# Kernel optimization log

Measured on AMD Instinct MI355X. Metric: run time of the kernel, lower is better.

The kernel has to match this reference:

```python
import jax, jax.numpy as jnp
import numpy as np

N, IN_DIM, OUT_DIM = 16384, 256, 128

def setup_inputs() -> dict:
    key = jax.random.key(0)
    ks = jax.random.split(key, 7)
    s_in = 1.0 / np.sqrt(IN_DIM)
    return {
        "x": jax.random.normal(ks[0], (N, IN_DIM), dtype=jnp.float32),
        "Wq": jax.random.uniform(ks[1], (IN_DIM, OUT_DIM), jnp.float32, -s_in, s_in),
        "bq": jax.random.uniform(ks[2], (OUT_DIM,), jnp.float32, -s_in, s_in),
        "Wk": jax.random.uniform(ks[3], (IN_DIM, OUT_DIM), jnp.float32, -s_in, s_in),
        "bk": jax.random.uniform(ks[4], (OUT_DIM,), jnp.float32, -s_in, s_in),
        "Wv": jax.random.uniform(ks[5], (IN_DIM, OUT_DIM), jnp.float32, -s_in, s_in),
        "bv": jax.random.uniform(ks[6], (OUT_DIM,), jnp.float32, -s_in, s_in),
    }

def reference(x, Wq, bq, Wk, bk, Wv, bv):
    # QKV projections: [N, out_dim]
    q = x @ Wq + bq
    k = x @ Wk + bk
    v = x @ Wv + bv
    # Unscaled dot-product affinity [N, N], row softmax, weighted sum of V.
    affinity = jax.nn.softmax(q @ k.T, axis=-1)
    return affinity @ v
```

## Files before the change

### kernel.cpp

```cpp
#include <hip/hip_runtime.h>

typedef _Float16 f16;
typedef _Float16 f16x8 __attribute__((ext_vector_type(8)));
typedef float f32x4 __attribute__((ext_vector_type(4)));
typedef float f32x16 __attribute__((ext_vector_type(16)));
typedef unsigned uint2v __attribute__((ext_vector_type(2)));

#define MFMA16(a, b, c) __builtin_amdgcn_mfma_f32_16x16x32_f16((a), (b), (c), 0, 0, 0)
#define MFMA32(a, b, c) __builtin_amdgcn_mfma_f32_32x32x16_f16((a), (b), (c), 0, 0, 0)
#define LOG2E 1.44269504088896340736f
#define SHIFT_L2 28.8539008178f

#define GLOAD_LDS16(g, l)                                              \
    __builtin_amdgcn_global_load_lds(                                  \
        (const __attribute__((address_space(1))) void*)(g),            \
        (__attribute__((address_space(3))) void*)(l), 16, 0, 0)

#define NROWS 16384
#define INDIM 256
#define ODIM 128
#define NQT 128

__global__ __launch_bounds__(256) void prep_kernel(
    const float* __restrict__ Wq, const float* __restrict__ Wk, const float* __restrict__ Wv,
    f16* __restrict__ WqT, f16* __restrict__ WkT, f16* __restrict__ WvT) {
    int w = blockIdx.x >> 5;
    int local = blockIdx.x & 31;
    const float* W = (w == 0) ? Wq : ((w == 1) ? Wk : Wv);
    f16* WT = (w == 0) ? WqT : ((w == 1) ? WkT : WvT);
    int j0 = local * 1024 + threadIdx.x;
#pragma unroll
    for (int t = 0; t < 4; t++) {
        int j = j0 + t * 256;
        int n = j >> 8;
        int k = j & 255;
        WT[j] = (f16)W[k * ODIM + n];
    }
}

__global__ __launch_bounds__(256) void proj_kernel(
    const float* __restrict__ x,
    const f16* __restrict__ WqT, const f16* __restrict__ WkT, const f16* __restrict__ WvT,
    const float* __restrict__ bq, const float* __restrict__ bk, const float* __restrict__ bv,
    f16* __restrict__ Qh, f16* __restrict__ Kh, f16* __restrict__ Vt) {
    int blk = blockIdx.x;
    int wave = threadIdx.x >> 6;
    int lane = threadIdx.x & 63;
    int l16 = lane & 15, quad = lane >> 4;

    int r0 = (blk & 255) * 64 + wave * 16;
    int c0 = (blk >> 8) * 64;

    f16x8 ax[8];
    const float* xp = x + (size_t)(r0 + l16) * INDIM + quad * 8;
#pragma unroll
    for (int kc = 0; kc < 8; kc++) {
        f32x4 u = *(const f32x4*)(xp + kc * 32);
        f32x4 v = *(const f32x4*)(xp + kc * 32 + 4);
        f16x8 t;
        t[0] = (f16)u[0]; t[1] = (f16)u[1]; t[2] = (f16)u[2]; t[3] = (f16)u[3];
        t[4] = (f16)v[0]; t[5] = (f16)v[1]; t[6] = (f16)v[2]; t[7] = (f16)v[3];
        ax[kc] = t;
    }
#pragma unroll
    for (int nt = 0; nt < 4; nt++) {
        int colb = c0 + nt * 16;
        f32x4 aq = {0.f, 0.f, 0.f, 0.f}, ak = {0.f, 0.f, 0.f, 0.f};
        f32x4 av = {0.f, 0.f, 0.f, 0.f};
        const f16* wq = WqT + (colb + l16) * INDIM + quad * 8;
        const f16* wk = WkT + (colb + l16) * INDIM + quad * 8;
        const f16* wv = WvT + (colb + l16) * INDIM + quad * 8;
#pragma unroll
        for (int kc = 0; kc < 8; kc++) {
            f16x8 bqf = *(const f16x8*)(wq + kc * 32);
            f16x8 bkf = *(const f16x8*)(wk + kc * 32);
            f16x8 avf = *(const f16x8*)(wv + kc * 32);
            aq = MFMA16(ax[kc], bqf, aq);
            ak = MFMA16(ax[kc], bkf, ak);
            av = MFMA16(avf, ax[kc], av);
        }
        int col = colb + l16;
        float biasq = bq[col], biask = bk[col];
#pragma unroll
        for (int r = 0; r < 4; r++) {
            int row = r0 + quad * 4 + r;
            Qh[(size_t)row * ODIM + col] = (f16)(aq[r] + biasq);
            Kh[(size_t)row * ODIM + col] = (f16)(ak[r] + biask);
            int d = colb + quad * 4 + r;
            Vt[(size_t)d * NROWS + r0 + l16] = (f16)(av[r] + bv[d]);
        }
    }
}

__global__ __launch_bounds__(256, 2) void flash_kernel(
    const f16* __restrict__ Qh, const f16* __restrict__ Kh, const f16* __restrict__ Vt,
    float* __restrict__ Opart, float* __restrict__ lbuf, float* __restrict__ Out,
    int nsplit, int niter) {
    int blk = blockIdx.x;
    int qt = blk & (NQT - 1);
    int sp = blk >> 7;
    int tid = threadIdx.x;
    int wave = tid >> 6;
    int lane = tid & 63;
    int l32 = lane & 31;
    int h = lane >> 5;

    __shared__ __align__(16) f16 Kl[2][64 * 128];
    __shared__ __align__(16) f16 Vl[2][128 * 64];

    int rowbase = qt * 128 + wave * 32;

    f16x8 qf[8];
    {
        const f16* qp = Qh + (size_t)(rowbase + l32) * ODIM + h * 8;
#pragma unroll
        for (int ks = 0; ks < 8; ks++) qf[ks] = *(const f16x8*)(qp + ks * 16);
    }

    f32x16 o[4];
#pragma unroll
    for (int dt = 0; dt < 4; dt++)
#pragma unroll
        for (int g = 0; g < 16; g++) o[dt][g] = 0.f;
    float l_r = 0.f;

    int rK[4], cK[4], dV[4], cV[4];
#pragma unroll
    for (int t = 0; t < 4; t++) {
        int s = wave * 256 + t * 64 + lane;
        rK[t] = s >> 4;
        cK[t] = ((s & 15) ^ (rK[t] & 7)) * 8;
        dV[t] = s >> 3;
        cV[t] = ((s & 7) ^ (dV[t] & 7)) * 8;
    }
    int rr = (l32 >> 1) & 3;
    int hh = h ^ (l32 & 1);

    int j0 = sp * (niter * 64);

#pragma unroll
    for (int t = 0; t < 4; t++) {
        GLOAD_LDS16(Kh + (size_t)(j0 + rK[t]) * ODIM + cK[t],
                    &Kl[0][(wave * 4 + t) * 512]);
        GLOAD_LDS16(Vt + (size_t)dV[t] * NROWS + j0 + cV[t],
                    &Vl[0][(wave * 4 + t) * 512]);
    }
    __syncthreads();

    for (int it = 0; it < niter; ++it) {
        int p = it & 1;
        if (it + 1 < niter) {
            int jn = j0 + 64;
#pragma unroll
            for (int t = 0; t < 4; t++) {
                GLOAD_LDS16(Kh + (size_t)(jn + rK[t]) * ODIM + cK[t],
                            &Kl[1 - p][(wave * 4 + t) * 512]);
                GLOAD_LDS16(Vt + (size_t)dV[t] * NROWS + jn + cV[t],
                            &Vl[1 - p][(wave * 4 + t) * 512]);
            }
        }
        int pk[2][8];
#pragma unroll
        for (int ct = 0; ct < 2; ct++) {
            f32x16 st;
#pragma unroll
            for (int g = 0; g < 16; g++) st[g] = 0.f;
            const f16* kb = &Kl[p][(ct * 32 + l32) * 128 + hh * 8];
#pragma unroll
            for (int ks = 0; ks < 8; ks++) {
                f16x8 kf = *(const f16x8*)(kb + ((ks ^ rr) << 4));
                st = MFMA32(kf, qf[ks], st);
            }
#pragma unroll
            for (int w = 0; w < 8; w++) {
                float a = __builtin_amdgcn_exp2f(fmaf(st[2 * w], LOG2E, -SHIFT_L2));
                float b = __builtin_amdgcn_exp2f(fmaf(st[2 * w + 1], LOG2E, -SHIFT_L2));
                l_r += a + b;
                pk[ct][w] = __builtin_bit_cast(int, __builtin_amdgcn_cvt_pkrtz(a, b));
            }
        }
        f16x8 pf[4];
#if __has_builtin(__builtin_amdgcn_permlane32_swap)
#pragma unroll
        for (int ks = 0; ks < 4; ks++) {
            int ct = ks >> 1, b = (ks & 1) * 4;
            uint2v r02 = __builtin_amdgcn_permlane32_swap(
                (unsigned)pk[ct][b], (unsigned)pk[ct][b + 2], false, false);
            uint2v r13 = __builtin_amdgcn_permlane32_swap(
                (unsigned)pk[ct][b + 1], (unsigned)pk[ct][b + 3], false, false);
            union { unsigned i[4]; f16x8 v; } u;
            u.i[0] = r02.x;
            u.i[1] = r13.x;
            u.i[2] = r02.y;
            u.i[3] = r13.y;
            pf[ks] = u.v;
        }
#else
#pragma unroll
        for (int ks = 0; ks < 4; ks++) {
            int ct = ks >> 1, b = (ks & 1) * 4;
            int off0 = h ? pk[ct][b] : pk[ct][b + 2];
            int off1 = h ? pk[ct][b + 1] : pk[ct][b + 3];
            int R0 = __shfl_xor(off0, 32, 64);
            int R1 = __shfl_xor(off1, 32, 64);
            union { int i[4]; f16x8 v; } u;
            u.i[0] = h ? R0 : pk[ct][b];
            u.i[1] = h ? R1 : pk[ct][b + 1];
            u.i[2] = h ? pk[ct][b + 2] : R0;
            u.i[3] = h ? pk[ct][b + 3] : R1;
            pf[ks] = u.v;
        }
#endif
#pragma unroll
        for (int dt = 0; dt < 4; dt++) {
            const f16* vb = &Vl[p][(dt * 32 + l32) * 64 + hh * 8];
#pragma unroll
            for (int ks = 0; ks < 4; ks++) {
                f16x8 vf = *(const f16x8*)(vb + ((ks ^ rr) << 4));
                o[dt] = MFMA32(vf, pf[ks], o[dt]);
            }
        }
        __syncthreads();
        j0 += 64;
    }

    l_r += __shfl_xor(l_r, 32, 64);

    if (nsplit == 1) {
        float inv = 1.f / l_r;
        float* op = Out + (size_t)(rowbase + l32) * ODIM;
#pragma unroll
        for (int dt = 0; dt < 4; dt++)
#pragma unroll
            for (int gg = 0; gg < 4; gg++) {
                f32x4 v = {o[dt][4 * gg] * inv, o[dt][4 * gg + 1] * inv,
                           o[dt][4 * gg + 2] * inv, o[dt][4 * gg + 3] * inv};
                *(f32x4*)(op + dt * 32 + 8 * gg + 4 * h) = v;
            }
    } else {
        float* op = Opart + ((size_t)sp * NROWS + rowbase + l32) * ODIM;
#pragma unroll
        for (int dt = 0; dt < 4; dt++)
#pragma unroll
            for (int gg = 0; gg < 4; gg++) {
                f32x4 v = {o[dt][4 * gg], o[dt][4 * gg + 1],
                           o[dt][4 * gg + 2], o[dt][4 * gg + 3]};
                *(f32x4*)(op + dt * 32 + 8 * gg + 4 * h) = v;
            }
        if (lane < 32)
            lbuf[(size_t)sp * NROWS + rowbase + l32] = l_r;
    }
}

__global__ __launch_bounds__(256) void merge_kernel(const float* __restrict__ Opart,
                                                    const float* __restrict__ lbuf,
                                                    float* __restrict__ out, int nsplit) {
    int idx = (blockIdx.x * 256 + threadIdx.x) * 4;
    int row = idx >> 7;
    f32x4 acc = {0.f, 0.f, 0.f, 0.f};
    float den = 0.f;
    for (int s = 0; s < nsplit; s++) {
        f32x4 v = *(const f32x4*)(Opart + (size_t)s * (NROWS * ODIM) + idx);
        acc[0] += v[0]; acc[1] += v[1]; acc[2] += v[2]; acc[3] += v[3];
        den += lbuf[(size_t)s * NROWS + row];
    }
    float inv = 1.f / den;
    f32x4 r = {acc[0] * inv, acc[1] * inv, acc[2] * inv, acc[3] * inv};
    *(f32x4*)(out + idx) = r;
}

extern "C" void kernel_launch(void* const* d_in, const int* in_sizes, int n_in,
                              void* d_out, int out_size, void* d_ws, size_t ws_size,
                              hipStream_t stream) {
    const float* x  = (const float*)d_in[0];
    const float* Wq = (const float*)d_in[1];
    const float* bq = (const float*)d_in[2];
    const float* Wk = (const float*)d_in[3];
    const float* bk = (const float*)d_in[4];
    const float* Wv = (const float*)d_in[5];
    const float* bv = (const float*)d_in[6];
    float* out = (float*)d_out;
    char* ws = (char*)d_ws;

    const size_t WT_BYTES = (size_t)ODIM * INDIM * sizeof(f16);
    const size_t QKV_BYTES = (size_t)NROWS * ODIM * sizeof(f16);
    f16* WqT = (f16*)(ws);
    f16* WkT = (f16*)(ws + WT_BYTES);
    f16* WvT = (f16*)(ws + 2 * WT_BYTES);
    f16* Qh  = (f16*)(ws + 3 * WT_BYTES);
    f16* Kh  = (f16*)(ws + 3 * WT_BYTES + QKV_BYTES);
    f16* Vt  = (f16*)(ws + 3 * WT_BYTES + 2 * QKV_BYTES);
    size_t base = 3 * WT_BYTES + 3 * QKV_BYTES;

    const size_t OPART_BYTES = (size_t)NROWS * ODIM * sizeof(float);
    const size_t L_BYTES = (size_t)NROWS * sizeof(float);

    int nsplit = 1;
    if (ws_size >= base + 4 * (OPART_BYTES + L_BYTES)) nsplit = 4;
    else if (ws_size >= base + 2 * (OPART_BYTES + L_BYTES)) nsplit = 2;

    float* Opart = (float*)(ws + base);
    float* lbuf  = (float*)(ws + base + (size_t)nsplit * OPART_BYTES);

    prep_kernel<<<96, 256, 0, stream>>>(Wq, Wk, Wv, WqT, WkT, WvT);
    proj_kernel<<<512, 256, 0, stream>>>(x, WqT, WkT, WvT, bq, bk, bv, Qh, Kh, Vt);
    flash_kernel<<<NQT * nsplit, 256, 0, stream>>>(Qh, Kh, Vt, Opart, lbuf, out, nsplit,
                                                   (NROWS / 64) / nsplit);
    if (nsplit > 1)
        merge_kernel<<<(NROWS * ODIM) / 1024, 256, 0, stream>>>(Opart, lbuf, out, nsplit);
}
```

Baseline: 244.6 us.

## Fuse prep, projection, flash and merge into one cooperative persistent kernel

Combines the four kernel launches into a single cooperative mega-kernel of 512 blocks that uses grid-wide syncs between the weight-transpose, QKV-projection, split flash-attention and merge phases. The aim is to remove launch gaps and per-kernel tail effects. In exchange it depends on cooperative launch support and on all 512 blocks being co-resident at two blocks per CU. The shared LDS allocation and the launch bounds of the flash phase now also apply to the lighter phases. If the cooperative launch fails, it falls back to the separate kernels.

```diff
diff --git a/kernel.cpp b/kernel.cpp
--- a/kernel.cpp
+++ b/kernel.cpp
@@ -1,4 +1,5 @@
 #include <hip/hip_runtime.h>
+#include <hip/hip_cooperative_groups.h>
 
 typedef _Float16 f16;
 typedef _Float16 f16x8 __attribute__((ext_vector_type(8)));
@@ -21,31 +22,26 @@
 #define ODIM 128
 #define NQT 128
 
-__global__ __launch_bounds__(256) void prep_kernel(
+__device__ __forceinline__ void prep_body(int gidx,
     const float* __restrict__ Wq, const float* __restrict__ Wk, const float* __restrict__ Wv,
     f16* __restrict__ WqT, f16* __restrict__ WkT, f16* __restrict__ WvT) {
-    int w = blockIdx.x >> 5;
-    int local = blockIdx.x & 31;
-    const float* W = (w == 0) ? Wq : ((w == 1) ? Wk : Wv);
-    f16* WT = (w == 0) ? WqT : ((w == 1) ? WkT : WvT);
-    int j0 = local * 1024 + threadIdx.x;
-#pragma unroll
-    for (int t = 0; t < 4; t++) {
-        int j = j0 + t * 256;
-        int n = j >> 8;
-        int k = j & 255;
+    if (gidx < 3 * 32768) {
+        int m = gidx >> 15;
+        int j = gidx & 32767;
+        const float* W = (m == 0) ? Wq : ((m == 1) ? Wk : Wv);
+        f16* WT = (m == 0) ? WqT : ((m == 1) ? WkT : WvT);
+        int n = j >> 8, k = j & 255;
         WT[j] = (f16)W[k * ODIM + n];
     }
 }
 
-__global__ __launch_bounds__(256) void proj_kernel(
+__device__ __forceinline__ void proj_body(int blk, int tid,
     const float* __restrict__ x,
     const f16* __restrict__ WqT, const f16* __restrict__ WkT, const f16* __restrict__ WvT,
     const float* __restrict__ bq, const float* __restrict__ bk, const float* __restrict__ bv,
     f16* __restrict__ Qh, f16* __restrict__ Kh, f16* __restrict__ Vt) {
-    int blk = blockIdx.x;
-    int wave = threadIdx.x >> 6;
-    int lane = threadIdx.x & 63;
+    int wave = tid >> 6;
+    int lane = tid & 63;
     int l16 = lane & 15, quad = lane >> 4;
 
     int r0 = (blk & 255) * 64 + wave * 16;
@@ -92,21 +88,20 @@
     }
 }
 
-__global__ __launch_bounds__(256, 2) void flash_kernel(
+__device__ __forceinline__ void flash_body(int blk, int tid,
+    f16* Kl0, f16* Kl1, f16* Vl0, f16* Vl1,
     const f16* __restrict__ Qh, const f16* __restrict__ Kh, const f16* __restrict__ Vt,
     float* __restrict__ Opart, float* __restrict__ lbuf, float* __restrict__ Out,
     int nsplit, int niter) {
-    int blk = blockIdx.x;
     int qt = blk & (NQT - 1);
     int sp = blk >> 7;
-    int tid = threadIdx.x;
     int wave = tid >> 6;
     int lane = tid & 63;
     int l32 = lane & 31;
     int h = lane >> 5;
 
-    __shared__ __align__(16) f16 Kl[2][64 * 128];
-    __shared__ __align__(16) f16 Vl[2][128 * 64];
+    f16* KlB[2] = {Kl0, Kl1};
+    f16* VlB[2] = {Vl0, Vl1};
 
     int rowbase = qt * 128 + wave * 32;
 
@@ -141,9 +136,9 @@
 #pragma unroll
     for (int t = 0; t < 4; t++) {
         GLOAD_LDS16(Kh + (size_t)(j0 + rK[t]) * ODIM + cK[t],
-                    &Kl[0][(wave * 4 + t) * 512]);
+                    &KlB[0][(wave * 4 + t) * 512]);
         GLOAD_LDS16(Vt + (size_t)dV[t] * NROWS + j0 + cV[t],
-                    &Vl[0][(wave * 4 + t) * 512]);
+                    &VlB[0][(wave * 4 + t) * 512]);
     }
     __syncthreads();
 
@@ -154,9 +149,9 @@
 #pragma unroll
             for (int t = 0; t < 4; t++) {
                 GLOAD_LDS16(Kh + (size_t)(jn + rK[t]) * ODIM + cK[t],
-                            &Kl[1 - p][(wave * 4 + t) * 512]);
+                            &KlB[1 - p][(wave * 4 + t) * 512]);
                 GLOAD_LDS16(Vt + (size_t)dV[t] * NROWS + jn + cV[t],
-                            &Vl[1 - p][(wave * 4 + t) * 512]);
+                            &VlB[1 - p][(wave * 4 + t) * 512]);
             }
         }
         int pk[2][8];
@@ -165,7 +160,7 @@
             f32x16 st;
 #pragma unroll
             for (int g = 0; g < 16; g++) st[g] = 0.f;
-            const f16* kb = &Kl[p][(ct * 32 + l32) * 128 + hh * 8];
+            const f16* kb = &KlB[p][(ct * 32 + l32) * 128 + hh * 8];
 #pragma unroll
             for (int ks = 0; ks < 8; ks++) {
                 f16x8 kf = *(const f16x8*)(kb + ((ks ^ rr) << 4));
@@ -213,7 +208,7 @@
 #endif
 #pragma unroll
         for (int dt = 0; dt < 4; dt++) {
-            const f16* vb = &Vl[p][(dt * 32 + l32) * 64 + hh * 8];
+            const f16* vb = &VlB[p][(dt * 32 + l32) * 64 + hh * 8];
 #pragma unroll
             for (int ks = 0; ks < 4; ks++) {
                 f16x8 vf = *(const f16x8*)(vb + ((ks ^ rr) << 4));
@@ -252,10 +247,9 @@
     }
 }
 
-__global__ __launch_bounds__(256) void merge_kernel(const float* __restrict__ Opart,
-                                                    const float* __restrict__ lbuf,
-                                                    float* __restrict__ out, int nsplit) {
-    int idx = (blockIdx.x * 256 + threadIdx.x) * 4;
+__device__ __forceinline__ void merge_body(int idx, int nsplit,
+    const float* __restrict__ Opart, const float* __restrict__ lbuf,
+    float* __restrict__ out) {
     int row = idx >> 7;
     f32x4 acc = {0.f, 0.f, 0.f, 0.f};
     float den = 0.f;
@@ -267,6 +261,70 @@
     float inv = 1.f / den;
     f32x4 r = {acc[0] * inv, acc[1] * inv, acc[2] * inv, acc[3] * inv};
     *(f32x4*)(out + idx) = r;
+}
+
+__global__ __launch_bounds__(256, 2) void mega_kernel(
+    const float* __restrict__ x,
+    const float* __restrict__ Wq, const float* __restrict__ bq,
+    const float* __restrict__ Wk, const float* __restrict__ bk,
+    const float* __restrict__ Wv, const float* __restrict__ bv,
+    f16* WqT, f16* WkT, f16* WvT, f16* Qh, f16* Kh, f16* Vt,
+    float* Opart, float* lbuf, float* out) {
+    __shared__ __align__(16) f16 Kl[2][64 * 128];
+    __shared__ __align__(16) f16 Vl[2][128 * 64];
+
+    cooperative_groups::grid_group grid = cooperative_groups::this_grid();
+    int blk = blockIdx.x;
+    int tid = threadIdx.x;
+
+    prep_body(blk * 256 + tid, Wq, Wk, Wv, WqT, WkT, WvT);
+    __threadfence();
+    grid.sync();
+
+    proj_body(blk, tid, x, WqT, WkT, WvT, bq, bk, bv, Qh, Kh, Vt);
+    __threadfence();
+    grid.sync();
+
+    flash_body(blk, tid, Kl[0], Kl[1], Vl[0], Vl[1],
+               Qh, Kh, Vt, Opart, lbuf, out, 4, 64);
+    __threadfence();
+    grid.sync();
+
+#pragma unroll
+    for (int i = 0; i < 4; i++) {
+        int idx = (blk * 256 + tid) * 4 + i * (512 * 256 * 4);
+        merge_body(idx, 4, Opart, lbuf, out);
+    }
+}
+
+__global__ __launch_bounds__(256) void prep_kernel(
+    const float* __restrict__ Wq, const float* __restrict__ Wk, const float* __restrict__ Wv,
+    f16* __restrict__ WqT, f16* __restrict__ WkT, f16* __restrict__ WvT) {
+    prep_body(blockIdx.x * 256 + threadIdx.x, Wq, Wk, Wv, WqT, WkT, WvT);
+}
+
+__global__ __launch_bounds__(256) void proj_kernel(
+    const float* __restrict__ x,
+    const f16* __restrict__ WqT, const f16* __restrict__ WkT, const f16* __restrict__ WvT,
+    const float* __restrict__ bq, const float* __restrict__ bk, const float* __restrict__ bv,
+    f16* __restrict__ Qh, f16* __restrict__ Kh, f16* __restrict__ Vt) {
+    proj_body(blockIdx.x, threadIdx.x, x, WqT, WkT, WvT, bq, bk, bv, Qh, Kh, Vt);
+}
+
+__global__ __launch_bounds__(256, 2) void flash_kernel(
+    const f16* __restrict__ Qh, const f16* __restrict__ Kh, const f16* __restrict__ Vt,
+    float* __restrict__ Opart, float* __restrict__ lbuf, float* __restrict__ Out,
+    int nsplit, int niter) {
+    __shared__ __align__(16) f16 Kl[2][64 * 128];
+    __shared__ __align__(16) f16 Vl[2][128 * 64];
+    flash_body(blockIdx.x, threadIdx.x, Kl[0], Kl[1], Vl[0], Vl[1],
+               Qh, Kh, Vt, Opart, lbuf, Out, nsplit, niter);
+}
+
+__global__ __launch_bounds__(256) void merge_kernel(const float* __restrict__ Opart,
+                                                    const float* __restrict__ lbuf,
+                                                    float* __restrict__ out, int nsplit) {
+    merge_body((blockIdx.x * 256 + threadIdx.x) * 4, nsplit, Opart, lbuf, out);
 }
 
 extern "C" void kernel_launch(void* const* d_in, const int* in_sizes, int n_in,
@@ -295,6 +353,18 @@
     const size_t OPART_BYTES = (size_t)NROWS * ODIM * sizeof(float);
     const size_t L_BYTES = (size_t)NROWS * sizeof(float);
 
+    bool coop_ok = (ws_size >= base + 4 * (OPART_BYTES + L_BYTES));
+
+    if (coop_ok) {
+        float* Opart = (float*)(ws + base);
+        float* lbuf  = (float*)(ws + base + 4 * OPART_BYTES);
+        void* args[] = {&x, &Wq, &bq, &Wk, &bk, &Wv, &bv,
+                        &WqT, &WkT, &WvT, &Qh, &Kh, &Vt, &Opart, &lbuf, &out};
+        hipError_t err = hipLaunchCooperativeKernel(
+            (const void*)mega_kernel, dim3(512), dim3(256), args, 0, stream);
+        if (err == hipSuccess) return;
+    }
+
     int nsplit = 1;
     if (ws_size >= base + 4 * (OPART_BYTES + L_BYTES)) nsplit = 4;
     else if (ws_size >= base + 2 * (OPART_BYTES + L_BYTES)) nsplit = 2;
@@ -302,7 +372,7 @@
     float* Opart = (float*)(ws + base);
     float* lbuf  = (float*)(ws + base + (size_t)nsplit * OPART_BYTES);
 
-    prep_kernel<<<96, 256, 0, stream>>>(Wq, Wk, Wv, WqT, WkT, WvT);
+    prep_kernel<<<512, 256, 0, stream>>>(Wq, Wk, Wv, WqT, WkT, WvT);
     proj_kernel<<<512, 256, 0, stream>>>(x, WqT, WkT, WvT, bq, bk, bv, Qh, Kh, Vt);
     flash_kernel<<<NQT * nsplit, 256, 0, stream>>>(Qh, Kh, Vt, Opart, lbuf, out, nsplit,
                                                    (NROWS / 64) / nsplit);
```

New measurement: 629.9 us. 2.58x slower.
